# Kernel tuning notes

Hardware: AMD Instinct MI355X
Metric: run time of the kernel (lower is better)

The kernel has to match this reference:

```python
import jax, jax.numpy as jnp
import numpy as np

APPERTURE = 256
LN_EPS = 1e-3  # keras LayerNormalization default


def _layernorm(x, gamma, beta):
    mu = jnp.mean(x, axis=-1, keepdims=True)
    var = jnp.mean(jnp.square(x - mu), axis=-1, keepdims=True)
    return (x - mu) * jax.lax.rsqrt(var + LN_EPS) * gamma + beta


def setup_inputs() -> dict:
    key = jax.random.key(0)
    ks = jax.random.split(key, 8)
    n, d = 4096, 1024
    s = 0.02
    return {
        "x": jax.random.normal(ks[0], (1, n, d), jnp.float32),
        "wk": s * jax.random.normal(ks[1], (d, d), jnp.float32),
        "wq": s * jax.random.normal(ks[2], (d, d), jnp.float32),
        "wv": s * jax.random.normal(ks[3], (d, d), jnp.float32),
        "wo": s * jax.random.normal(ks[4], (d, d), jnp.float32),
        "wka": s * jax.random.normal(ks[5], (d, d), jnp.float32),
        "bka": jnp.zeros((d,), jnp.float32),
        "wkd": s * jax.random.normal(ks[6], (d, 1), jnp.float32),
        "bkd": jnp.zeros((1,), jnp.float32),
        "g_y": jnp.ones((d,), jnp.float32),
        "b_y": jnp.zeros((d,), jnp.float32),
        "g_ka": jnp.ones((d,), jnp.float32),
        "b_ka": jnp.zeros((d,), jnp.float32),
    }


def reference(x, wk, wq, wv, wo, wka, bka, wkd, bkd, g_y, b_y, g_ka, b_ka):
    m = x.shape[2]
    xf = x.reshape(-1, m)            # (n, m); seqlen == max_seqlen so no pad/trunc
    n = xf.shape[0]
    K = xf @ wk                      # (n, d)
    Q = (xf @ wq) * 0.06             # (n, d)
    V = xf @ wv                      # (n, d)
    logits = Q @ K.T                 # (n, n)
    # banded (apperture) mask: entries with |i-j| > apperture -> -inf
    idx = jnp.arange(n)
    band = jnp.abs(idx[:, None] - idx[None, :]) <= APPERTURE
    logits = jnp.where(band, logits, -jnp.inf)
    weights = jax.nn.softmax(logits, axis=0)   # softmax over queries (axis 0), as in original
    # y = transpose(V^T @ W) = W^T @ V
    y = weights.T @ V                # (n, d)
    y = y @ wo + xf                  # output_linear (no bias) + residual
    y = _layernorm(y, g_y, b_y)
    y = jax.nn.relu(y @ wka + bka)
    y = _layernorm(y, g_ka, b_ka)
    y = jax.nn.sigmoid(y @ wkd + bkd)  # (n, 1)
    return y.reshape(1, -1)            # (1, n)
```

## Files before the change

kernel.cpp:

```cpp
#include <hip/hip_runtime.h>
#include <hip/hip_bf16.h>
#include <math.h>

typedef __hip_bfloat16 bf16;
typedef __attribute__((ext_vector_type(8))) short bf16x8;
typedef __attribute__((ext_vector_type(4))) float f32x4;

#define NROW 4096
#define DIM  1024
#define APP  256
#define WIN  640
#define VTPW 4608

__device__ __forceinline__ unsigned short f2bu(float f) {
    bf16 h = __float2bfloat16(f);
    return *reinterpret_cast<unsigned short*>(&h);
}
__device__ __forceinline__ float bu2f(unsigned short u) {
    bf16 h; *reinterpret_cast<unsigned short*>(&h) = u;
    return __bfloat162float(h);
}
__device__ __forceinline__ unsigned pk2(float a, float b) {
    return (unsigned)f2bu(a) | ((unsigned)f2bu(b) << 16);
}
__device__ __forceinline__ void gload_lds16(const void* g, void* l) {
    __builtin_amdgcn_global_load_lds(
        (const __attribute__((address_space(1))) unsigned int*)g,
        (__attribute__((address_space(3))) unsigned int*)l, 16, 0, 0);
}

struct PrepArgs { const float* x; bf16* xb; const float* srcw[5]; bf16* dstw[5]; bf16* Vtp; };
__global__ __launch_bounds__(256) void prep_kernel(PrepArgs p) {
    __shared__ float T[64][65];
    const int bid = blockIdx.x, t = threadIdx.x;
    if (bid < 2048) {
        size_t base = ((size_t)bid * 256 + t) * 8;
        float4 v0 = *(const float4*)(p.x + base);
        float4 v1 = *(const float4*)(p.x + base + 4);
        uint4 o;
        o.x = pk2(v0.x, v0.y); o.y = pk2(v0.z, v0.w);
        o.z = pk2(v1.x, v1.y); o.w = pk2(v1.z, v1.w);
        *(uint4*)(p.xb + base) = o;
        return;
    }
    if (bid < 3328) {
        int r = bid - 2048;
        const int z = r >> 8; r &= 255;
        const int r0 = (r & 15) * 64, c0 = (r >> 4) * 64;
        const float* in = p.srcw[z];
        bf16* out = p.dstw[z];
        if (z < 3) {
            #pragma unroll
            for (int c = 0; c < 4; ++c) {
                int row = (t >> 4) + c * 16, col = (t & 15) * 4;
                float4 v = *(const float4*)(in + (size_t)(r0 + row) * 1024 + c0 + col);
                uint2 o; o.x = pk2(v.x, v.y); o.y = pk2(v.z, v.w);
                *(uint2*)(out + (size_t)(r0 + row) * 1024 + c0 + col) = o;
            }
            return;
        }
        #pragma unroll
        for (int c = 0; c < 4; ++c) {
            int row = (t >> 4) + c * 16, col = (t & 15) * 4;
            float4 v = *(const float4*)(in + (size_t)(r0 + row) * 1024 + c0 + col);
            T[row][col] = v.x; T[row][col + 1] = v.y; T[row][col + 2] = v.z; T[row][col + 3] = v.w;
        }
        __syncthreads();
        #pragma unroll
        for (int c = 0; c < 4; ++c) {
            int orow = (t >> 4) + c * 16, ocol = (t & 15) * 4;
            uint2 o;
            o.x = pk2(T[ocol][orow], T[ocol + 1][orow]);
            o.y = pk2(T[ocol + 2][orow], T[ocol + 3][orow]);
            *(uint2*)(out + (size_t)(c0 + orow) * 1024 + r0 + ocol) = o;
        }
        return;
    }
    {
        int idx = (bid - 3328) * 256 + t;
        int row = idx >> 7;
        int c4  = idx & 127;
        int col = (c4 < 64) ? (c4 * 4) : (4352 + (c4 - 64) * 4);
        *(uint2*)(p.Vtp + (size_t)row * VTPW + col) = (uint2){0u, 0u};
    }
}

template <int BM, int BN>
__global__ __launch_bounds__(256) void gemm_bt(
    const bf16* __restrict__ A, int lda, const bf16* __restrict__ Bt, int ldb,
    bf16* __restrict__ C, int ldc, int K,
    float alpha, const float* __restrict__ bias, int relu, int pv)
{
    constexpr int WM = BM / 2, WN = BN / 2, AI = WM / 16, BJ = WN / 16;
    __shared__ bf16 As[BM * 64];
    __shared__ bf16 Bs[BN * 64];
    const int t = threadIdx.x, l = t & 63, w = t >> 6;
    const int wr = w >> 1, wc = w & 1;
    const int jl = l & 15, g = l >> 4;
    const int m0 = blockIdx.y * BM, n0 = blockIdx.x * BN;
    const bf16* Btb = pv ? (Bt + (size_t)(m0 >> 7) * 128) : Bt;

    f32x4 acc[AI][BJ];
    #pragma unroll
    for (int i = 0; i < AI; ++i)
        #pragma unroll
        for (int j = 0; j < BJ; ++j) acc[i][j] = (f32x4){0.f, 0.f, 0.f, 0.f};

    for (int kk = 0; kk < K; kk += 64) {
        __syncthreads();
        #pragma unroll
        for (int c = 0; c < BM / 32; ++c) {
            int q = t + c * 256;
            int row = q >> 3;
            int kel = ((q & 7) ^ (row & 7)) << 3;
            gload_lds16(A + (size_t)(m0 + row) * lda + kk + kel,
                        (char*)As + (c * 256 + w * 64) * 16);
        }
        #pragma unroll
        for (int c = 0; c < BN / 32; ++c) {
            int q = t + c * 256;
            int row = q >> 3;
            int kel = ((q & 7) ^ (row & 7)) << 3;
            gload_lds16(Btb + (size_t)(n0 + row) * ldb + kk + kel,
                        (char*)Bs + (c * 256 + w * 64) * 16);
        }
        __syncthreads();
        #pragma unroll
        for (int ks = 0; ks < 2; ++ks) {
            bf16x8 af[AI], bfr[BJ];
            #pragma unroll
            for (int i = 0; i < AI; ++i) {
                int ra = wr * WM + i * 16 + jl;
                af[i] = *(const bf16x8*)((char*)As + ra * 128 + ((ks * 64 + g * 16) ^ ((ra & 7) << 4)));
            }
            #pragma unroll
            for (int j = 0; j < BJ; ++j) {
                int rb = wc * WN + j * 16 + jl;
                bfr[j] = *(const bf16x8*)((char*)Bs + rb * 128 + ((ks * 64 + g * 16) ^ ((rb & 7) << 4)));
            }
            #pragma unroll
            for (int i = 0; i < AI; ++i)
                #pragma unroll
                for (int j = 0; j < BJ; ++j)
                    acc[i][j] = __builtin_amdgcn_mfma_f32_16x16x32_bf16(af[i], bfr[j], acc[i][j], 0, 0, 0);
        }
    }

    const int g4 = g * 4;
    #pragma unroll
    for (int j = 0; j < BJ; ++j) {
        int col = n0 + wc * WN + j * 16 + jl;
        float bv = bias ? bias[col] : 0.f;
        #pragma unroll
        for (int i = 0; i < AI; ++i) {
            int rowb = m0 + wr * WM + i * 16 + g4;
            #pragma unroll
            for (int r = 0; r < 4; ++r) {
                float vv = alpha * acc[i][j][r] + bv;
                if (relu) vv = fmaxf(vv, 0.f);
                C[(size_t)(rowb + r) * ldc + col] = __float2bfloat16(vv);
            }
        }
    }
}

struct MiniPtrs { const bf16* A[2]; const bf16* Bt[2]; bf16* C[2]; };
__global__ __launch_bounds__(256) void gemm_mini(MiniPtrs p) {
    constexpr int WM = 32, WN = 32, AI = 2, BJ = 2;
    __shared__ bf16 As[64 * 64];
    __shared__ bf16 Bs[64 * 64];
    const bf16* A  = p.A[blockIdx.z];
    const bf16* Bt = p.Bt[blockIdx.z];
    bf16* C        = p.C[blockIdx.z];
    const int t = threadIdx.x, l = t & 63, w = t >> 6;
    const int wr = w >> 1, wc = w & 1;
    const int jl = l & 15, g = l >> 4;
    const int m0 = blockIdx.y * 64, n0 = blockIdx.x * 64;

    f32x4 acc[AI][BJ];
    #pragma unroll
    for (int i = 0; i < AI; ++i)
        #pragma unroll
        for (int j = 0; j < BJ; ++j) acc[i][j] = (f32x4){0.f, 0.f, 0.f, 0.f};

    for (int kk = 0; kk < DIM; kk += 64) {
        __syncthreads();
        #pragma unroll
        for (int c = 0; c < 2; ++c) {
            int q = t + c * 256;
            int row = q >> 3;
            int kel = ((q & 7) ^ (row & 7)) << 3;
            gload_lds16(A + (size_t)(m0 + row) * DIM + kk + kel,
                        (char*)As + (c * 256 + w * 64) * 16);
            gload_lds16(Bt + (size_t)(n0 + row) * DIM + kk + kel,
                        (char*)Bs + (c * 256 + w * 64) * 16);
        }
        __syncthreads();
        #pragma unroll
        for (int ks = 0; ks < 2; ++ks) {
            bf16x8 af[AI], bfr[BJ];
            #pragma unroll
            for (int i = 0; i < AI; ++i) {
                int ra = wr * WM + i * 16 + jl;
                af[i] = *(const bf16x8*)((char*)As + ra * 128 + ((ks * 64 + g * 16) ^ ((ra & 7) << 4)));
            }
            #pragma unroll
            for (int j = 0; j < BJ; ++j) {
                int rb = wc * WN + j * 16 + jl;
                bfr[j] = *(const bf16x8*)((char*)Bs + rb * 128 + ((ks * 64 + g * 16) ^ ((rb & 7) << 4)));
            }
            #pragma unroll
            for (int i = 0; i < AI; ++i)
                #pragma unroll
                for (int j = 0; j < BJ; ++j)
                    acc[i][j] = __builtin_amdgcn_mfma_f32_16x16x32_bf16(af[i], bfr[j], acc[i][j], 0, 0, 0);
        }
    }

    const int g4 = g * 4;
    #pragma unroll
    for (int j = 0; j < BJ; ++j) {
        int col = n0 + wc * WN + j * 16 + jl;
        #pragma unroll
        for (int i = 0; i < AI; ++i) {
            int rowb = m0 + wr * WM + i * 16 + g4;
            #pragma unroll
            for (int r = 0; r < 4; ++r)
                C[(size_t)(rowb + r) * DIM + col] = __float2bfloat16(acc[i][j][r]);
        }
    }
}

__global__ __launch_bounds__(256) void score_gemm(const bf16* __restrict__ Qh,
                                                  const bf16* __restrict__ xb,
                                                  bf16* __restrict__ St)
{
    constexpr int WM = 32, WN = 64, AI = 2, BJ = 4;
    __shared__ bf16 As[64 * 64];
    __shared__ bf16 Bs[128 * 64];
    const int t = threadIdx.x, l = t & 63, w = t >> 6;
    const int wr = w >> 1, wc = w & 1;
    const int jl = l & 15, g = l >> 4;
    const int tt = blockIdx.y;
    const int c0 = blockIdx.x * 64;
    const int win0 = tt * 128 - APP;
    const bf16* Kb = xb + (size_t)tt * 128 * DIM;

    f32x4 acc[AI][BJ];
    #pragma unroll
    for (int i = 0; i < AI; ++i)
        #pragma unroll
        for (int j = 0; j < BJ; ++j) acc[i][j] = (f32x4){0.f, 0.f, 0.f, 0.f};

    for (int kk = 0; kk < DIM; kk += 64) {
        __syncthreads();
        #pragma unroll
        for (int c = 0; c < 2; ++c) {
            int q = t + c * 256;
            int row = q >> 3;
            int kel = ((q & 7) ^ (row & 7)) << 3;
            int rg = win0 + c0 + row;
            rg = min(max(rg, 0), NROW - 1);
            gload_lds16(Qh + (size_t)rg * DIM + kk + kel,
                        (char*)As + (c * 256 + w * 64) * 16);
        }
        #pragma unroll
        for (int c = 0; c < 4; ++c) {
            int q = t + c * 256;
            int row = q >> 3;
            int kel = ((q & 7) ^ (row & 7)) << 3;
            gload_lds16(Kb + (size_t)row * DIM + kk + kel,
                        (char*)Bs + (c * 256 + w * 64) * 16);
        }
        __syncthreads();
        #pragma unroll
        for (int ks = 0; ks < 2; ++ks) {
            bf16x8 af[AI], bfr[BJ];
            #pragma unroll
            for (int i = 0; i < AI; ++i) {
                int ra = wr * WM + i * 16 + jl;
                af[i] = *(const bf16x8*)((char*)As + ra * 128 + ((ks * 64 + g * 16) ^ ((ra & 7) << 4)));
            }
            #pragma unroll
            for (int j = 0; j < BJ; ++j) {
                int rb = wc * WN + j * 16 + jl;
                bfr[j] = *(const bf16x8*)((char*)Bs + rb * 128 + ((ks * 64 + g * 16) ^ ((rb & 7) << 4)));
            }
            #pragma unroll
            for (int i = 0; i < AI; ++i)
                #pragma unroll
                for (int j = 0; j < BJ; ++j)
                    acc[i][j] = __builtin_amdgcn_mfma_f32_16x16x32_bf16(af[i], bfr[j], acc[i][j], 0, 0, 0);
        }
    }

    const int g4 = g * 4;
    #pragma unroll
    for (int j = 0; j < BJ; ++j) {
        int coll = wc * WN + j * 16 + jl;
        bf16* strow = St + (size_t)(tt * 128 + coll) * WIN;
        #pragma unroll
        for (int i = 0; i < AI; ++i) {
            int iwb = c0 + wr * WM + i * 16 + g4;
            #pragma unroll
            for (int r = 0; r < 4; ++r)
                strow[iwb + r] = __float2bfloat16(0.06f * acc[i][j][r]);
        }
    }
}

__global__ __launch_bounds__(256) void softmax_band(bf16* __restrict__ St)
{
    const int w = threadIdx.x >> 6, l = threadIdx.x & 63;
    const int j = blockIdx.x * 4 + w;
    const int tt = j >> 7, jt = j & 127;
    unsigned* row = (unsigned*)(St + (size_t)j * WIN);
    const int lo = max(jt, 256 - 128 * tt);
    const int hi = min(jt + 512, 4351 - 128 * tt);
    unsigned u[5]; float v[10];
    #pragma unroll
    for (int c = 0; c < 5; ++c) u[c] = row[l + 64 * c];
    float m = -3e38f;
    #pragma unroll
    for (int c = 0; c < 5; ++c) {
        int iw = 2 * (l + 64 * c);
        v[2 * c]     = (iw >= lo && iw <= hi)         ? bu2f((unsigned short)(u[c] & 0xffff)) : -3e38f;
        v[2 * c + 1] = (iw + 1 >= lo && iw + 1 <= hi) ? bu2f((unsigned short)(u[c] >> 16))    : -3e38f;
        m = fmaxf(m, fmaxf(v[2 * c], v[2 * c + 1]));
    }
    #pragma unroll
    for (int off = 32; off > 0; off >>= 1) m = fmaxf(m, __shfl_xor(m, off));
    float s = 0.f;
    #pragma unroll
    for (int c = 0; c < 10; ++c) {
        float e = (v[c] > -1e37f) ? __expf(v[c] - m) : 0.f;
        v[c] = e; s += e;
    }
    #pragma unroll
    for (int off = 32; off > 0; off >>= 1) s += __shfl_xor(s, off);
    const float inv = 1.f / s;
    #pragma unroll
    for (int c = 0; c < 5; ++c)
        row[l + 64 * c] = pk2(v[2 * c] * inv, v[2 * c + 1] * inv);
}

__global__ __launch_bounds__(256) void ln_kernel(
    const bf16* __restrict__ T, const float* __restrict__ X,
    const float* __restrict__ g, const float* __restrict__ b, bf16* __restrict__ O)
{
    __shared__ float red1[4], red2[4];
    const int r = blockIdx.x, t = threadIdx.x, lane = t & 63, w = t >> 6;
    ushort4 tv = ((const ushort4*)(T + (size_t)r * DIM))[t];
    float v0 = bu2f(tv.x), v1 = bu2f(tv.y), v2 = bu2f(tv.z), v3 = bu2f(tv.w);
    if (X) {
        float4 xv = ((const float4*)(X + (size_t)r * DIM))[t];
        v0 += xv.x; v1 += xv.y; v2 += xv.z; v3 += xv.w;
    }
    float s = v0 + v1 + v2 + v3;
    #pragma unroll
    for (int off = 32; off > 0; off >>= 1) s += __shfl_xor(s, off);
    if (lane == 0) red1[w] = s;
    __syncthreads();
    float mu = (red1[0] + red1[1] + red1[2] + red1[3]) * (1.f / DIM);
    float d0 = v0 - mu, d1 = v1 - mu, d2 = v2 - mu, d3 = v3 - mu;
    float s2 = d0 * d0 + d1 * d1 + d2 * d2 + d3 * d3;
    #pragma unroll
    for (int off = 32; off > 0; off >>= 1) s2 += __shfl_xor(s2, off);
    if (lane == 0) red2[w] = s2;
    __syncthreads();
    float var = (red2[0] + red2[1] + red2[2] + red2[3]) * (1.f / DIM);
    float rstd = rsqrtf(var + 1e-3f);
    float4 gv = ((const float4*)g)[t];
    float4 bv = ((const float4*)b)[t];
    uint2 o;
    o.x = pk2(d0 * rstd * gv.x + bv.x, d1 * rstd * gv.y + bv.y);
    o.y = pk2(d2 * rstd * gv.z + bv.z, d3 * rstd * gv.w + bv.w);
    ((uint2*)(O + (size_t)r * DIM))[t] = o;
}

__global__ __launch_bounds__(256) void lnfinal_kernel(
    const bf16* __restrict__ T, const float* __restrict__ g, const float* __restrict__ b,
    const float* __restrict__ wkd, const float* __restrict__ bkd, float* __restrict__ out)
{
    __shared__ float red1[4], red2[4], red3[4];
    const int r = blockIdx.x, t = threadIdx.x, lane = t & 63, w = t >> 6;
    ushort4 tv = ((const ushort4*)(T + (size_t)r * DIM))[t];
    float v0 = bu2f(tv.x), v1 = bu2f(tv.y), v2 = bu2f(tv.z), v3 = bu2f(tv.w);
    float s = v0 + v1 + v2 + v3;
    #pragma unroll
    for (int off = 32; off > 0; off >>= 1) s += __shfl_xor(s, off);
    if (lane == 0) red1[w] = s;
    __syncthreads();
    float mu = (red1[0] + red1[1] + red1[2] + red1[3]) * (1.f / DIM);
    float d0 = v0 - mu, d1 = v1 - mu, d2 = v2 - mu, d3 = v3 - mu;
    float s2 = d0 * d0 + d1 * d1 + d2 * d2 + d3 * d3;
    #pragma unroll
    for (int off = 32; off > 0; off >>= 1) s2 += __shfl_xor(s2, off);
    if (lane == 0) red2[w] = s2;
    __syncthreads();
    float var = (red2[0] + red2[1] + red2[2] + red2[3]) * (1.f / DIM);
    float rstd = rsqrtf(var + 1e-3f);
    float4 gv = ((const float4*)g)[t];
    float4 bv = ((const float4*)b)[t];
    float4 wv = ((const float4*)wkd)[t];
    float s3 = (d0 * rstd * gv.x + bv.x) * wv.x + (d1 * rstd * gv.y + bv.y) * wv.y
             + (d2 * rstd * gv.z + bv.z) * wv.z + (d3 * rstd * gv.w + bv.w) * wv.w;
    #pragma unroll
    for (int off = 32; off > 0; off >>= 1) s3 += __shfl_xor(s3, off);
    if (lane == 0) red3[w] = s3;
    __syncthreads();
    if (t == 0) {
        float tot = red3[0] + red3[1] + red3[2] + red3[3];
        out[r] = 1.f / (1.f + __expf(-(tot + bkd[0])));
    }
}

extern "C" void kernel_launch(void* const* d_in, const int* in_sizes, int n_in,
                              void* d_out, int out_size, void* d_ws, size_t ws_size,
                              hipStream_t stream) {
    const float* x    = (const float*)d_in[0];
    const float* wk   = (const float*)d_in[1];
    const float* wq   = (const float*)d_in[2];
    const float* wv   = (const float*)d_in[3];
    const float* wo   = (const float*)d_in[4];
    const float* wka  = (const float*)d_in[5];
    const float* bka  = (const float*)d_in[6];
    const float* wkd  = (const float*)d_in[7];
    const float* bkd  = (const float*)d_in[8];
    const float* g_y  = (const float*)d_in[9];
    const float* b_y  = (const float*)d_in[10];
    const float* g_ka = (const float*)d_in[11];
    const float* b_ka = (const float*)d_in[12];
    float* out = (float*)d_out;

    char* ws = (char*)d_ws;
    const size_t MB = 1u << 20;
    bf16* wkB  = (bf16*)(ws);
    bf16* wqB  = (bf16*)(ws + 2 * MB);
    bf16* wvB  = (bf16*)(ws + 4 * MB);
    bf16* woT  = (bf16*)(ws + 6 * MB);
    bf16* wkaT = (bf16*)(ws + 8 * MB);
    bf16* WqkT = (bf16*)(ws + 10 * MB);
    bf16* wvoT = (bf16*)(ws + 12 * MB);
    bf16* xb   = (bf16*)(ws + 14 * MB);
    bf16* Qh   = (bf16*)(ws + 22 * MB);
    bf16* Vtp  = (bf16*)(ws + 30 * MB);
    bf16* St   = (bf16*)(ws + 40 * MB);
    bf16* fT   = (bf16*)(ws + 46 * MB);
    bf16* fL1  = (bf16*)(ws + 54 * MB);
    bf16* fRel = (bf16*)(ws + 62 * MB);

    PrepArgs pa;
    pa.x = x; pa.xb = xb; pa.Vtp = Vtp;
    pa.srcw[0] = wk;  pa.srcw[1] = wq;  pa.srcw[2] = wv;  pa.srcw[3] = wo;  pa.srcw[4] = wka;
    pa.dstw[0] = wkB; pa.dstw[1] = wqB; pa.dstw[2] = wvB; pa.dstw[3] = woT; pa.dstw[4] = wkaT;
    prep_kernel<<<3840, 256, 0, stream>>>(pa);

    MiniPtrs mp;
    mp.A[0] = wkB; mp.Bt[0] = wqB; mp.C[0] = WqkT;
    mp.A[1] = woT; mp.Bt[1] = wvB; mp.C[1] = wvoT;
    gemm_mini<<<dim3(16, 16, 2), 256, 0, stream>>>(mp);

    gemm_bt<128, 64><<<dim3(16, 32), 256, 0, stream>>>(
        xb, DIM, WqkT, DIM, Qh, DIM, DIM, 1.f, nullptr, 0, 0);
    gemm_bt<64, 128><<<dim3(32, 16), 256, 0, stream>>>(
        wvoT, DIM, xb, DIM, Vtp + 256, VTPW, DIM, 1.f, nullptr, 0, 0);

    score_gemm<<<dim3(WIN / 64, NROW / 128), 256, 0, stream>>>(Qh, xb, St);
    softmax_band<<<NROW / 4, 256, 0, stream>>>(St);
    gemm_bt<64, 128><<<dim3(8, 64), 256, 0, stream>>>(
        St, WIN, Vtp, VTPW, fT, DIM, WIN, 1.f, nullptr, 0, 1);

    ln_kernel<<<NROW, 256, 0, stream>>>(fT, x, g_y, b_y, fL1);
    gemm_bt<128, 64><<<dim3(16, 32), 256, 0, stream>>>(
        fL1, DIM, wkaT, DIM, fRel, DIM, DIM, 1.f, bka, 1, 0);
    lnfinal_kernel<<<NROW, 256, 0, stream>>>(fRel, g_ka, b_ka, wkd, bkd, out);
}
```

Before: 124.4 us.

## Fuse Q and V projections into one wide GEMM and transpose V separately

The separate Q projection and transposed-V projection GEMMs become one 4096x2048 GEMM with 128x128 tiles. It reads the two adjacent weight buffers (WqkT, wvoT) as a single 2048-row operand. A new tiled LDS transpose kernel then scatters the V half into the padded transposed Vtp layout that the attention GEMM expects. gemm_mini is retiled to 128x64, and the LayerNorm residual now reads the bf16 copy of x instead of fp32. The aim is to cut launch count and improve GEMM efficiency, at the cost of an extra transpose pass and slightly lower residual precision.

New measurement: 123.2 us. Within noise of the previous version (-1.0%).

```diff
diff --git a/kernel.cpp b/kernel.cpp
--- a/kernel.cpp
+++ b/kernel.cpp
@@ -11,6 +11,7 @@
 #define APP  256
 #define WIN  640
 #define VTPW 4608
+#define OLD  2048
 
 __device__ __forceinline__ unsigned short f2bu(float f) {
     bf16 h = __float2bfloat16(f);
@@ -166,16 +167,16 @@
 
 struct MiniPtrs { const bf16* A[2]; const bf16* Bt[2]; bf16* C[2]; };
 __global__ __launch_bounds__(256) void gemm_mini(MiniPtrs p) {
-    constexpr int WM = 32, WN = 32, AI = 2, BJ = 2;
-    __shared__ bf16 As[64 * 64];
-    __shared__ bf16 Bs[64 * 64];
+    constexpr int BM = 128, BN = 64, WM = 64, WN = 32, AI = 4, BJ = 2;
+    __shared__ bf16 As[BM * 64];
+    __shared__ bf16 Bs[BN * 64];
     const bf16* A  = p.A[blockIdx.z];
     const bf16* Bt = p.Bt[blockIdx.z];
     bf16* C        = p.C[blockIdx.z];
     const int t = threadIdx.x, l = t & 63, w = t >> 6;
     const int wr = w >> 1, wc = w & 1;
     const int jl = l & 15, g = l >> 4;
-    const int m0 = blockIdx.y * 64, n0 = blockIdx.x * 64;
+    const int m0 = blockIdx.y * BM, n0 = blockIdx.x * BN;
 
     f32x4 acc[AI][BJ];
     #pragma unroll
@@ -186,12 +187,18 @@
     for (int kk = 0; kk < DIM; kk += 64) {
         __syncthreads();
         #pragma unroll
-        for (int c = 0; c < 2; ++c) {
+        for (int c = 0; c < BM / 32; ++c) {
             int q = t + c * 256;
             int row = q >> 3;
             int kel = ((q & 7) ^ (row & 7)) << 3;
             gload_lds16(A + (size_t)(m0 + row) * DIM + kk + kel,
                         (char*)As + (c * 256 + w * 64) * 16);
+        }
+        #pragma unroll
+        for (int c = 0; c < BN / 32; ++c) {
+            int q = t + c * 256;
+            int row = q >> 3;
+            int kel = ((q & 7) ^ (row & 7)) << 3;
             gload_lds16(Bt + (size_t)(n0 + row) * DIM + kk + kel,
                         (char*)Bs + (c * 256 + w * 64) * 16);
         }
@@ -228,6 +235,32 @@
             for (int r = 0; r < 4; ++r)
                 C[(size_t)(rowb + r) * DIM + col] = __float2bfloat16(acc[i][j][r]);
         }
+    }
+}
+
+__global__ __launch_bounds__(256) void tpad_kernel(const bf16* __restrict__ O,
+                                                   bf16* __restrict__ Vtp)
+{
+    __shared__ unsigned short T[64][65];
+    const int t = threadIdx.x;
+    const int j0 = blockIdx.x * 64, d0 = blockIdx.y * 64;
+    #pragma unroll
+    for (int c = 0; c < 4; ++c) {
+        int row = (t >> 4) + c * 16, col = (t & 15) * 4;
+        uint2 v = *(const uint2*)(O + (size_t)(j0 + row) * OLD + 1024 + d0 + col);
+        T[row][col]     = (unsigned short)(v.x & 0xffff);
+        T[row][col + 1] = (unsigned short)(v.x >> 16);
+        T[row][col + 2] = (unsigned short)(v.y & 0xffff);
+        T[row][col + 3] = (unsigned short)(v.y >> 16);
+    }
+    __syncthreads();
+    #pragma unroll
+    for (int c = 0; c < 4; ++c) {
+        int orow = (t >> 4) + c * 16, ocol = (t & 15) * 4;
+        uint2 o;
+        o.x = (unsigned)T[ocol][orow]     | ((unsigned)T[ocol + 1][orow] << 16);
+        o.y = (unsigned)T[ocol + 2][orow] | ((unsigned)T[ocol + 3][orow] << 16);
+        *(uint2*)(Vtp + (size_t)(d0 + orow) * VTPW + 256 + j0 + ocol) = o;
     }
 }
 
@@ -261,7 +294,7 @@
             int kel = ((q & 7) ^ (row & 7)) << 3;
             int rg = win0 + c0 + row;
             rg = min(max(rg, 0), NROW - 1);
-            gload_lds16(Qh + (size_t)rg * DIM + kk + kel,
+            gload_lds16(Qh + (size_t)rg * OLD + kk + kel,
                         (char*)As + (c * 256 + w * 64) * 16);
         }
         #pragma unroll
@@ -345,16 +378,16 @@
 }
 
 __global__ __launch_bounds__(256) void ln_kernel(
-    const bf16* __restrict__ T, const float* __restrict__ X,
+    const bf16* __restrict__ T, const bf16* __restrict__ Xb,
     const float* __restrict__ g, const float* __restrict__ b, bf16* __restrict__ O)
 {
     __shared__ float red1[4], red2[4];
     const int r = blockIdx.x, t = threadIdx.x, lane = t & 63, w = t >> 6;
     ushort4 tv = ((const ushort4*)(T + (size_t)r * DIM))[t];
     float v0 = bu2f(tv.x), v1 = bu2f(tv.y), v2 = bu2f(tv.z), v3 = bu2f(tv.w);
-    if (X) {
-        float4 xv = ((const float4*)(X + (size_t)r * DIM))[t];
-        v0 += xv.x; v1 += xv.y; v2 += xv.z; v3 += xv.w;
+    if (Xb) {
+        ushort4 xv = ((const ushort4*)(Xb + (size_t)r * DIM))[t];
+        v0 += bu2f(xv.x); v1 += bu2f(xv.y); v2 += bu2f(xv.z); v3 += bu2f(xv.w);
     }
     float s = v0 + v1 + v2 + v3;
     #pragma unroll
@@ -443,12 +476,12 @@
     bf16* WqkT = (bf16*)(ws + 10 * MB);
     bf16* wvoT = (bf16*)(ws + 12 * MB);
     bf16* xb   = (bf16*)(ws + 14 * MB);
-    bf16* Qh   = (bf16*)(ws + 22 * MB);
-    bf16* Vtp  = (bf16*)(ws + 30 * MB);
-    bf16* St   = (bf16*)(ws + 40 * MB);
-    bf16* fT   = (bf16*)(ws + 46 * MB);
-    bf16* fL1  = (bf16*)(ws + 54 * MB);
-    bf16* fRel = (bf16*)(ws + 62 * MB);
+    bf16* Obuf = (bf16*)(ws + 22 * MB);
+    bf16* Vtp  = (bf16*)(ws + 38 * MB);
+    bf16* St   = (bf16*)(ws + 47 * MB);
+    bf16* fT   = (bf16*)(ws + 53 * MB);
+    bf16* fL1  = (bf16*)(ws + 61 * MB);
+    bf16* fRel = (bf16*)(ws + 69 * MB);
 
     PrepArgs pa;
     pa.x = x; pa.xb = xb; pa.Vtp = Vtp;
@@ -459,19 +492,18 @@
     MiniPtrs mp;
     mp.A[0] = wkB; mp.Bt[0] = wqB; mp.C[0] = WqkT;
     mp.A[1] = woT; mp.Bt[1] = wvB; mp.C[1] = wvoT;
-    gemm_mini<<<dim3(16, 16, 2), 256, 0, stream>>>(mp);
-
-    gemm_bt<128, 64><<<dim3(16, 32), 256, 0, stream>>>(
-        xb, DIM, WqkT, DIM, Qh, DIM, DIM, 1.f, nullptr, 0, 0);
-    gemm_bt<64, 128><<<dim3(32, 16), 256, 0, stream>>>(
-        wvoT, DIM, xb, DIM, Vtp + 256, VTPW, DIM, 1.f, nullptr, 0, 0);
-
-    score_gemm<<<dim3(WIN / 64, NROW / 128), 256, 0, stream>>>(Qh, xb, St);
+    gemm_mini<<<dim3(16, 8, 2), 256, 0, stream>>>(mp);
+
+    gemm_bt<128, 128><<<dim3(16, 32), 256, 0, stream>>>(
+        xb, DIM, WqkT, DIM, Obuf, OLD, DIM, 1.f, nullptr, 0, 0);
+    tpad_kernel<<<dim3(64, 16), 256, 0, stream>>>(Obuf, Vtp);
+
+    score_gemm<<<dim3(WIN / 64, NROW / 128), 256, 0, stream>>>(Obuf, xb, St);
     softmax_band<<<NROW / 4, 256, 0, stream>>>(St);
     gemm_bt<64, 128><<<dim3(8, 64), 256, 0, stream>>>(
         St, WIN, Vtp, VTPW, fT, DIM, WIN, 1.f, nullptr, 0, 1);
 
-    ln_kernel<<<NROW, 256, 0, stream>>>(fT, x, g_y, b_y, fL1);
+    ln_kernel<<<NROW, 256, 0, stream>>>(fT, xb, g_y, b_y, fL1);
     gemm_bt<128, 64><<<dim3(16, 32), 256, 0, stream>>>(
         fL1, DIM, wkaT, DIM, fRel, DIM, DIM, 1.f, bka, 1, 0);
     lnfinal_kernel<<<NROW, 256, 0, stream>>>(fRel, g_ka, b_ka, wkd, bkd, out);
```
